# Optimization experiments

Measured on AMD Instinct MI355X. Metric: run time of the kernel, lower is better.

## Reference

```python
import jax, jax.numpy as jnp
import numpy as np

N = 256        # num_nodes
F = 256        # feature_dim
B = 32         # batch
DEG = 32       # out-degree per node -> E = N*DEG edges


def setup_inputs() -> dict:
    key = jax.random.key(0)
    k1, k2, k3, k4 = jax.random.split(key, 4)
    node_features = jax.random.normal(k1, (B, N, F), dtype=jnp.float32)
    # xavier_uniform for [N, N, F] tensor: fan_in = N*F, fan_out = N*F per torch default flattening
    limit = float(np.sqrt(6.0 / (N * F + N * F)))
    W = jax.random.uniform(k2, (N, N, F), dtype=jnp.float32, minval=-limit, maxval=limit)
    phase = jax.random.uniform(k3, (N, N), dtype=jnp.float32, minval=0.0, maxval=2.0 * np.pi)
    # topology: each node i has DEG outgoing connections (paths[i])
    src = jnp.repeat(jnp.arange(N, dtype=jnp.int64), DEG)              # [E]
    dst = jax.random.randint(k4, (N * DEG,), 0, N, dtype=jnp.int64)    # [E]
    return {"node_features": node_features, "W": W, "phase": phase, "src": src, "dst": dst}


def reference(node_features, W, phase, src, dst):
    # real(exp(i*phase)) == cos(phase); per-edge effective weight [E, F]
    eff_w = W[src, dst, :] * jnp.cos(phase[src, dst])[:, None]
    # gather source node features and scale: [B, E, F]
    signal = node_features[:, src, :] * eff_w[None, :, :]
    # scatter-add into destination nodes
    propagated = jnp.zeros_like(node_features).at[:, dst, :].add(signal)
    # normalization by out-degree of each node index (matches original indexing)
    n = node_features.shape[1]
    counts = jnp.zeros((n,), dtype=node_features.dtype).at[src].add(1.0)
    norm = jnp.maximum(counts, 1.0)
    return propagated / norm[None, :, None]
```

## Files before the change

### kernel.cpp

```cpp
#include <hip/hip_runtime.h>
#include <math.h>

#define NN 256
#define FF 256
#define BB 32
#define EE 8192


#define FGROUPS 8
#define CAP 96

__global__ __launch_bounds__(256, 4) void fused_propagate_kernel(
    const float4* __restrict__ nf4,
    const float4* __restrict__ W4,
    const float*  __restrict__ phase,
    const int*    __restrict__ dst,
    float4*       __restrict__ out4)
{
    const int fg   = blockIdx.x & (FGROUPS - 1);
    const int d    = blockIdx.x >> 3;
    const int tid  = threadIdx.x;
    const int lane = tid & 63;
    const int wv   = tid >> 6;

    __shared__ int    scnt[NN];
    __shared__ int2   lsa[CAP];
    __shared__ int    wtot[4];
    __shared__ float4 aw4[CAP * 8];

    const int4* dstq = (const int4*)dst;
    int c[8];
    #pragma unroll
    for (int i = 0; i < 8; i++) {
        const int4 v = dstq[tid + 256 * i];
        c[i] = (v.x == d) + (v.y == d) + (v.z == d) + (v.w == d);
    }
    #pragma unroll
    for (int off = 1; off < 8; off <<= 1) {
        #pragma unroll
        for (int i = 0; i < 8; i++) c[i] += __shfl_xor(c[i], off, 64);
    }
    if ((tid & 7) == 0) {
        const int g = tid >> 3;
        #pragma unroll
        for (int i = 0; i < 8; i++) scnt[g + 32 * i] = c[i];
    }
    __syncthreads();

    const int cnt = scnt[tid];
    const int ind = (cnt > 0) ? 1 : 0;

    const unsigned long long mask  = __ballot(ind);
    const int                below = __popcll(mask & ((1ULL << lane) - 1ULL));
    if (lane == 0) wtot[wv] = __popcll(mask);
    __syncthreads();

    int wbase = 0;
    #pragma unroll
    for (int w = 0; w < 4; w++) wbase += (w < wv) ? wtot[w] : 0;
    const int total = wtot[0] + wtot[1] + wtot[2] + wtot[3];

    if (ind) {
        const float a = (float)cnt * cosf(phase[tid * NN + d]) * 0.03125f;
        lsa[wbase + below] = make_int2(tid, __float_as_int(a));
    }
    const int n4 = (total + 3) & ~3;
    if (tid < n4 - total) lsa[total + tid] = make_int2(0, 0);
    __syncthreads();

    const int wrow = d * (FF / 4) + fg * 8;
    for (int slot = tid; slot < n4 * 8; slot += 256) {
        const int  e = slot >> 3, f = slot & 7;
        const int2 sa = lsa[e];
        const float a = __int_as_float(sa.y);
        float4 w = W4[sa.x * (NN * FF / 4) + wrow + f];
        w.x *= a; w.y *= a; w.z *= a; w.w *= a;
        aw4[slot] = w;
    }
    __syncthreads();

    const int myf = tid & 7;
    const int b   = tid >> 3;
    const int nfb = b * (NN * FF / 4) + fg * 8 + myf;

    float4 acc = {0.f, 0.f, 0.f, 0.f};

    if (n4 > 0) {
        int s0 = lsa[0].x, s1 = lsa[1].x, s2 = lsa[2].x, s3 = lsa[3].x;
        float4 x0 = nf4[nfb + s0 * (FF / 4)];
        float4 x1 = nf4[nfb + s1 * (FF / 4)];
        float4 x2 = nf4[nfb + s2 * (FF / 4)];
        float4 x3 = nf4[nfb + s3 * (FF / 4)];

        for (int k = 4; k < n4; k += 4) {
            const int t0 = lsa[k + 0].x, t1 = lsa[k + 1].x;
            const int t2 = lsa[k + 2].x, t3 = lsa[k + 3].x;
            const float4 y0 = nf4[nfb + t0 * (FF / 4)];
            const float4 y1 = nf4[nfb + t1 * (FF / 4)];
            const float4 y2 = nf4[nfb + t2 * (FF / 4)];
            const float4 y3 = nf4[nfb + t3 * (FF / 4)];

            {
                const float4 a0 = aw4[(k - 4) * 8 + myf];
                const float4 a1 = aw4[(k - 3) * 8 + myf];
                const float4 a2 = aw4[(k - 2) * 8 + myf];
                const float4 a3 = aw4[(k - 1) * 8 + myf];
                acc.x = fmaf(x0.x, a0.x, acc.x); acc.y = fmaf(x0.y, a0.y, acc.y);
                acc.z = fmaf(x0.z, a0.z, acc.z); acc.w = fmaf(x0.w, a0.w, acc.w);
                acc.x = fmaf(x1.x, a1.x, acc.x); acc.y = fmaf(x1.y, a1.y, acc.y);
                acc.z = fmaf(x1.z, a1.z, acc.z); acc.w = fmaf(x1.w, a1.w, acc.w);
                acc.x = fmaf(x2.x, a2.x, acc.x); acc.y = fmaf(x2.y, a2.y, acc.y);
                acc.z = fmaf(x2.z, a2.z, acc.z); acc.w = fmaf(x2.w, a2.w, acc.w);
                acc.x = fmaf(x3.x, a3.x, acc.x); acc.y = fmaf(x3.y, a3.y, acc.y);
                acc.z = fmaf(x3.z, a3.z, acc.z); acc.w = fmaf(x3.w, a3.w, acc.w);
            }
            x0 = y0; x1 = y1; x2 = y2; x3 = y3;
        }

        {
            const float4 a0 = aw4[(n4 - 4) * 8 + myf];
            const float4 a1 = aw4[(n4 - 3) * 8 + myf];
            const float4 a2 = aw4[(n4 - 2) * 8 + myf];
            const float4 a3 = aw4[(n4 - 1) * 8 + myf];
            acc.x = fmaf(x0.x, a0.x, acc.x); acc.y = fmaf(x0.y, a0.y, acc.y);
            acc.z = fmaf(x0.z, a0.z, acc.z); acc.w = fmaf(x0.w, a0.w, acc.w);
            acc.x = fmaf(x1.x, a1.x, acc.x); acc.y = fmaf(x1.y, a1.y, acc.y);
            acc.z = fmaf(x1.z, a1.z, acc.z); acc.w = fmaf(x1.w, a1.w, acc.w);
            acc.x = fmaf(x2.x, a2.x, acc.x); acc.y = fmaf(x2.y, a2.y, acc.y);
            acc.z = fmaf(x2.z, a2.z, acc.z); acc.w = fmaf(x2.w, a2.w, acc.w);
            acc.x = fmaf(x3.x, a3.x, acc.x); acc.y = fmaf(x3.y, a3.y, acc.y);
            acc.z = fmaf(x3.z, a3.z, acc.z); acc.w = fmaf(x3.w, a3.w, acc.w);
        }
    }

    out4[b * (NN * FF / 4) + d * (FF / 4) + fg * 8 + myf] = acc;
}

extern "C" void kernel_launch(void* const* d_in, const int* in_sizes, int n_in,
                              void* d_out, int out_size, void* d_ws, size_t ws_size,
                              hipStream_t stream) {
    const float* nf    = (const float*)d_in[0];
    const float* W     = (const float*)d_in[1];
    const float* phase = (const float*)d_in[2];
    const int*   dst   = (const int*)d_in[4];
    float*       out   = (float*)d_out;

    fused_propagate_kernel<<<NN * FGROUPS, 256, 0, stream>>>(
        (const float4*)nf, (const float4*)W, phase, dst, (float4*)out);
}
```

Measured before the change: 116.0 us.

## Use one 1024-thread block per destination node covering all features

Replaces the 8 feature-group blocks per destination node with a single 1024-thread block per node that handles all 256 features. Each thread now accumulates two float4 outputs, and the destination histogram, compaction and phase lookups are done once per node rather than eight times. This removes redundant scanning of the dst array and lowers block count, but grid size drops to 256 blocks and shared memory per block grows to about 96 KB. That limits occupancy and may underfill the GPU's compute units.

```diff
diff --git a/kernel.cpp b/kernel.cpp
--- a/kernel.cpp
+++ b/kernel.cpp
@@ -7,18 +7,16 @@
 #define EE 8192
 
 
-#define FGROUPS 8
 #define CAP 96
 
-__global__ __launch_bounds__(256, 4) void fused_propagate_kernel(
+__global__ __launch_bounds__(1024, 4) void fused_propagate_kernel(
     const float4* __restrict__ nf4,
     const float4* __restrict__ W4,
     const float*  __restrict__ phase,
     const int*    __restrict__ dst,
     float4*       __restrict__ out4)
 {
-    const int fg   = blockIdx.x & (FGROUPS - 1);
-    const int d    = blockIdx.x >> 3;
+    const int d    = blockIdx.x;
     const int tid  = threadIdx.x;
     const int lane = tid & 63;
     const int wv   = tid >> 6;
@@ -26,39 +24,36 @@
     __shared__ int    scnt[NN];
     __shared__ int2   lsa[CAP];
     __shared__ int    wtot[4];
-    __shared__ float4 aw4[CAP * 8];
+    __shared__ float4 aw4[CAP * 64];
 
     const int4* dstq = (const int4*)dst;
-    int c[8];
-    #pragma unroll
-    for (int i = 0; i < 8; i++) {
-        const int4 v = dstq[tid + 256 * i];
-        c[i] = (v.x == d) + (v.y == d) + (v.z == d) + (v.w == d);
-    }
+    const int4 v0 = dstq[tid];
+    const int4 v1 = dstq[tid + 1024];
+    int c0 = (v0.x == d) + (v0.y == d) + (v0.z == d) + (v0.w == d);
+    int c1 = (v1.x == d) + (v1.y == d) + (v1.z == d) + (v1.w == d);
     #pragma unroll
     for (int off = 1; off < 8; off <<= 1) {
-        #pragma unroll
-        for (int i = 0; i < 8; i++) c[i] += __shfl_xor(c[i], off, 64);
+        c0 += __shfl_xor(c0, off, 64);
+        c1 += __shfl_xor(c1, off, 64);
     }
     if ((tid & 7) == 0) {
-        const int g = tid >> 3;
-        #pragma unroll
-        for (int i = 0; i < 8; i++) scnt[g + 32 * i] = c[i];
+        scnt[tid >> 3]       = c0;
+        scnt[128 + (tid >> 3)] = c1;
     }
     __syncthreads();
 
-    const int cnt = scnt[tid];
-    const int ind = (cnt > 0) ? 1 : 0;
+    int cnt = 0, ind = 0;
+    if (tid < NN) { cnt = scnt[tid]; ind = (cnt > 0) ? 1 : 0; }
 
     const unsigned long long mask  = __ballot(ind);
     const int                below = __popcll(mask & ((1ULL << lane) - 1ULL));
-    if (lane == 0) wtot[wv] = __popcll(mask);
+    if (wv < 4 && lane == 0) wtot[wv] = __popcll(mask);
     __syncthreads();
 
+    const int total = wtot[0] + wtot[1] + wtot[2] + wtot[3];
     int wbase = 0;
     #pragma unroll
     for (int w = 0; w < 4; w++) wbase += (w < wv) ? wtot[w] : 0;
-    const int total = wtot[0] + wtot[1] + wtot[2] + wtot[3];
 
     if (ind) {
         const float a = (float)cnt * cosf(phase[tid * NN + d]) * 0.03125f;
@@ -68,72 +63,107 @@
     if (tid < n4 - total) lsa[total + tid] = make_int2(0, 0);
     __syncthreads();
 
-    const int wrow = d * (FF / 4) + fg * 8;
-    for (int slot = tid; slot < n4 * 8; slot += 256) {
-        const int  e = slot >> 3, f = slot & 7;
+    const int drow = d * (FF / 4);
+    for (int slot = tid; slot < n4 * 64; slot += 1024) {
+        const int  e = slot >> 6, f = slot & 63;
         const int2 sa = lsa[e];
         const float a = __int_as_float(sa.y);
-        float4 w = W4[sa.x * (NN * FF / 4) + wrow + f];
+        float4 w = W4[sa.x * (NN * FF / 4) + drow + f];
         w.x *= a; w.y *= a; w.z *= a; w.w *= a;
         aw4[slot] = w;
     }
     __syncthreads();
 
-    const int myf = tid & 7;
-    const int b   = tid >> 3;
-    const int nfb = b * (NN * FF / 4) + fg * 8 + myf;
+    const int b   = tid >> 5;
+    const int q   = tid & 31;
+    const int nfb = b * (NN * (FF / 4)) + q;
 
-    float4 acc = {0.f, 0.f, 0.f, 0.f};
+    float4 acc0 = {0.f, 0.f, 0.f, 0.f};
+    float4 acc1 = {0.f, 0.f, 0.f, 0.f};
 
     if (n4 > 0) {
         int s0 = lsa[0].x, s1 = lsa[1].x, s2 = lsa[2].x, s3 = lsa[3].x;
-        float4 x0 = nf4[nfb + s0 * (FF / 4)];
-        float4 x1 = nf4[nfb + s1 * (FF / 4)];
-        float4 x2 = nf4[nfb + s2 * (FF / 4)];
-        float4 x3 = nf4[nfb + s3 * (FF / 4)];
+        float4 xl0 = nf4[nfb + s0 * 64];
+        float4 xh0 = nf4[nfb + s0 * 64 + 32];
+        float4 xl1 = nf4[nfb + s1 * 64];
+        float4 xh1 = nf4[nfb + s1 * 64 + 32];
+        float4 xl2 = nf4[nfb + s2 * 64];
+        float4 xh2 = nf4[nfb + s2 * 64 + 32];
+        float4 xl3 = nf4[nfb + s3 * 64];
+        float4 xh3 = nf4[nfb + s3 * 64 + 32];
 
         for (int k = 4; k < n4; k += 4) {
             const int t0 = lsa[k + 0].x, t1 = lsa[k + 1].x;
             const int t2 = lsa[k + 2].x, t3 = lsa[k + 3].x;
-            const float4 y0 = nf4[nfb + t0 * (FF / 4)];
-            const float4 y1 = nf4[nfb + t1 * (FF / 4)];
-            const float4 y2 = nf4[nfb + t2 * (FF / 4)];
-            const float4 y3 = nf4[nfb + t3 * (FF / 4)];
+            const float4 yl0 = nf4[nfb + t0 * 64];
+            const float4 yh0 = nf4[nfb + t0 * 64 + 32];
+            const float4 yl1 = nf4[nfb + t1 * 64];
+            const float4 yh1 = nf4[nfb + t1 * 64 + 32];
+            const float4 yl2 = nf4[nfb + t2 * 64];
+            const float4 yh2 = nf4[nfb + t2 * 64 + 32];
+            const float4 yl3 = nf4[nfb + t3 * 64];
+            const float4 yh3 = nf4[nfb + t3 * 64 + 32];
 
             {
-                const float4 a0 = aw4[(k - 4) * 8 + myf];
-                const float4 a1 = aw4[(k - 3) * 8 + myf];
-                const float4 a2 = aw4[(k - 2) * 8 + myf];
-                const float4 a3 = aw4[(k - 1) * 8 + myf];
-                acc.x = fmaf(x0.x, a0.x, acc.x); acc.y = fmaf(x0.y, a0.y, acc.y);
-                acc.z = fmaf(x0.z, a0.z, acc.z); acc.w = fmaf(x0.w, a0.w, acc.w);
-                acc.x = fmaf(x1.x, a1.x, acc.x); acc.y = fmaf(x1.y, a1.y, acc.y);
-                acc.z = fmaf(x1.z, a1.z, acc.z); acc.w = fmaf(x1.w, a1.w, acc.w);
-                acc.x = fmaf(x2.x, a2.x, acc.x); acc.y = fmaf(x2.y, a2.y, acc.y);
-                acc.z = fmaf(x2.z, a2.z, acc.z); acc.w = fmaf(x2.w, a2.w, acc.w);
-                acc.x = fmaf(x3.x, a3.x, acc.x); acc.y = fmaf(x3.y, a3.y, acc.y);
-                acc.z = fmaf(x3.z, a3.z, acc.z); acc.w = fmaf(x3.w, a3.w, acc.w);
+                const float4 al0 = aw4[(k - 4) * 64 + q];
+                const float4 ah0 = aw4[(k - 4) * 64 + q + 32];
+                const float4 al1 = aw4[(k - 3) * 64 + q];
+                const float4 ah1 = aw4[(k - 3) * 64 + q + 32];
+                const float4 al2 = aw4[(k - 2) * 64 + q];
+                const float4 ah2 = aw4[(k - 2) * 64 + q + 32];
+                const float4 al3 = aw4[(k - 1) * 64 + q];
+                const float4 ah3 = aw4[(k - 1) * 64 + q + 32];
+                acc0.x = fmaf(xl0.x, al0.x, acc0.x); acc0.y = fmaf(xl0.y, al0.y, acc0.y);
+                acc0.z = fmaf(xl0.z, al0.z, acc0.z); acc0.w = fmaf(xl0.w, al0.w, acc0.w);
+                acc1.x = fmaf(xh0.x, ah0.x, acc1.x); acc1.y = fmaf(xh0.y, ah0.y, acc1.y);
+                acc1.z = fmaf(xh0.z, ah0.z, acc1.z); acc1.w = fmaf(xh0.w, ah0.w, acc1.w);
+                acc0.x = fmaf(xl1.x, al1.x, acc0.x); acc0.y = fmaf(xl1.y, al1.y, acc0.y);
+                acc0.z = fmaf(xl1.z, al1.z, acc0.z); acc0.w = fmaf(xl1.w, al1.w, acc0.w);
+                acc1.x = fmaf(xh1.x, ah1.x, acc1.x); acc1.y = fmaf(xh1.y, ah1.y, acc1.y);
+                acc1.z = fmaf(xh1.z, ah1.z, acc1.z); acc1.w = fmaf(xh1.w, ah1.w, acc1.w);
+                acc0.x = fmaf(xl2.x, al2.x, acc0.x); acc0.y = fmaf(xl2.y, al2.y, acc0.y);
+                acc0.z = fmaf(xl2.z, al2.z, acc0.z); acc0.w = fmaf(xl2.w, al2.w, acc0.w);
+                acc1.x = fmaf(xh2.x, ah2.x, acc1.x); acc1.y = fmaf(xh2.y, ah2.y, acc1.y);
+                acc1.z = fmaf(xh2.z, ah2.z, acc1.z); acc1.w = fmaf(xh2.w, ah2.w, acc1.w);
+                acc0.x = fmaf(xl3.x, al3.x, acc0.x); acc0.y = fmaf(xl3.y, al3.y, acc0.y);
+                acc0.z = fmaf(xl3.z, al3.z, acc0.z); acc0.w = fmaf(xl3.w, al3.w, acc0.w);
+                acc1.x = fmaf(xh3.x, ah3.x, acc1.x); acc1.y = fmaf(xh3.y, ah3.y, acc1.y);
+                acc1.z = fmaf(xh3.z, ah3.z, acc1.z); acc1.w = fmaf(xh3.w, ah3.w, acc1.w);
             }
-            x0 = y0; x1 = y1; x2 = y2; x3 = y3;
+            xl0 = yl0; xh0 = yh0; xl1 = yl1; xh1 = yh1;
+            xl2 = yl2; xh2 = yh2; xl3 = yl3; xh3 = yh3;
         }
 
         {
-            const float4 a0 = aw4[(n4 - 4) * 8 + myf];
-            const float4 a1 = aw4[(n4 - 3) * 8 + myf];
-            const float4 a2 = aw4[(n4 - 2) * 8 + myf];
-            const float4 a3 = aw4[(n4 - 1) * 8 + myf];
-            acc.x = fmaf(x0.x, a0.x, acc.x); acc.y = fmaf(x0.y, a0.y, acc.y);
-            acc.z = fmaf(x0.z, a0.z, acc.z); acc.w = fmaf(x0.w, a0.w, acc.w);
-            acc.x = fmaf(x1.x, a1.x, acc.x); acc.y = fmaf(x1.y, a1.y, acc.y);
-            acc.z = fmaf(x1.z, a1.z, acc.z); acc.w = fmaf(x1.w, a1.w, acc.w);
-            acc.x = fmaf(x2.x, a2.x, acc.x); acc.y = fmaf(x2.y, a2.y, acc.y);
-            acc.z = fmaf(x2.z, a2.z, acc.z); acc.w = fmaf(x2.w, a2.w, acc.w);
-            acc.x = fmaf(x3.x, a3.x, acc.x); acc.y = fmaf(x3.y, a3.y, acc.y);
-            acc.z = fmaf(x3.z, a3.z, acc.z); acc.w = fmaf(x3.w, a3.w, acc.w);
+            const float4 al0 = aw4[(n4 - 4) * 64 + q];
+            const float4 ah0 = aw4[(n4 - 4) * 64 + q + 32];
+            const float4 al1 = aw4[(n4 - 3) * 64 + q];
+            const float4 ah1 = aw4[(n4 - 3) * 64 + q + 32];
+            const float4 al2 = aw4[(n4 - 2) * 64 + q];
+            const float4 ah2 = aw4[(n4 - 2) * 64 + q + 32];
+            const float4 al3 = aw4[(n4 - 1) * 64 + q];
+            const float4 ah3 = aw4[(n4 - 1) * 64 + q + 32];
+            acc0.x = fmaf(xl0.x, al0.x, acc0.x); acc0.y = fmaf(xl0.y, al0.y, acc0.y);
+            acc0.z = fmaf(xl0.z, al0.z, acc0.z); acc0.w = fmaf(xl0.w, al0.w, acc0.w);
+            acc1.x = fmaf(xh0.x, ah0.x, acc1.x); acc1.y = fmaf(xh0.y, ah0.y, acc1.y);
+            acc1.z = fmaf(xh0.z, ah0.z, acc1.z); acc1.w = fmaf(xh0.w, ah0.w, acc1.w);
+            acc0.x = fmaf(xl1.x, al1.x, acc0.x); acc0.y = fmaf(xl1.y, al1.y, acc0.y);
+            acc0.z = fmaf(xl1.z, al1.z, acc0.z); acc0.w = fmaf(xl1.w, al1.w, acc0.w);
+            acc1.x = fmaf(xh1.x, ah1.x, acc1.x); acc1.y = fmaf(xh1.y, ah1.y, acc1.y);
+            acc1.z = fmaf(xh1.z, ah1.z, acc1.z); acc1.w = fmaf(xh1.w, ah1.w, acc1.w);
+            acc0.x = fmaf(xl2.x, al2.x, acc0.x); acc0.y = fmaf(xl2.y, al2.y, acc0.y);
+            acc0.z = fmaf(xl2.z, al2.z, acc0.z); acc0.w = fmaf(xl2.w, al2.w, acc0.w);
+            acc1.x = fmaf(xh2.x, ah2.x, acc1.x); acc1.y = fmaf(xh2.y, ah2.y, acc1.y);
+            acc1.z = fmaf(xh2.z, ah2.z, acc1.z); acc1.w = fmaf(xh2.w, ah2.w, acc1.w);
+            acc0.x = fmaf(xl3.x, al3.x, acc0.x); acc0.y = fmaf(xl3.y, al3.y, acc0.y);
+            acc0.z = fmaf(xl3.z, al3.z, acc0.z); acc0.w = fmaf(xl3.w, al3.w, acc0.w);
+            acc1.x = fmaf(xh3.x, ah3.x, acc1.x); acc1.y = fmaf(xh3.y, ah3.y, acc1.y);
+            acc1.z = fmaf(xh3.z, ah3.z, acc1.z); acc1.w = fmaf(xh3.w, ah3.w, acc1.w);
         }
     }
 
-    out4[b * (NN * FF / 4) + d * (FF / 4) + fg * 8 + myf] = acc;
+    out4[b * (NN * (FF / 4)) + drow + q]      = acc0;
+    out4[b * (NN * (FF / 4)) + drow + q + 32] = acc1;
 }
 
 extern "C" void kernel_launch(void* const* d_in, const int* in_sizes, int n_in,
@@ -145,6 +175,6 @@
     const int*   dst   = (const int*)d_in[4];
     float*       out   = (float*)d_out;
 
-    fused_propagate_kernel<<<NN * FGROUPS, 256, 0, stream>>>(
+    fused_propagate_kernel<<<NN, 1024, 0, stream>>>(
         (const float4*)nf, (const float4*)W, phase, dst, (float4*)out);
 }
```

Result: no change. 114.9 us (-1.0%).

## Stage node features in LDS per feature quad and process 64 destinations per block

Applied to the files above, without the earlier changes.

Each block now owns one float4 feature column across all batches and nodes, loading the full B×N slice of node features into LDS once and reusing it for 64 destination nodes. Edge counts are built with a packed-byte LDS histogram via atomics, and per-destination source/coef lists are compacted per wave. W is streamed directly from global memory with a one-step register prefetch instead of being prescaled in LDS. This cuts redundant global reads of node features, at the cost of 128KB LDS per block, 1024-thread blocks and only 256 blocks, and the per-destination source list is truncated at CAP entries.

```diff
diff --git a/kernel.cpp b/kernel.cpp
--- a/kernel.cpp
+++ b/kernel.cpp
@@ -5,135 +5,161 @@
 #define FF 256
 #define BB 32
 #define EE 8192
+#define F4  (FF / 4)
+#define NF4 (NN * F4)
 
 
-#define FGROUPS 8
-#define CAP 96
+#define CAP 80
 
-__global__ __launch_bounds__(256, 4) void fused_propagate_kernel(
+#define CONSUME4()                                                             \
+    {                                                                          \
+        const float4 xA = nf_lds[sA * 32 + b];                                 \
+        const float4 xB = nf_lds[sB * 32 + b];                                 \
+        const float4 xC = nf_lds[sC * 32 + b];                                 \
+        const float4 xD = nf_lds[sD * 32 + b];                                 \
+        float4 aw;                                                             \
+        aw.x = a4.x * wA.x; aw.y = a4.x * wA.y;                                \
+        aw.z = a4.x * wA.z; aw.w = a4.x * wA.w;                                \
+        acc.x = fmaf(xA.x, aw.x, acc.x); acc.y = fmaf(xA.y, aw.y, acc.y);      \
+        acc.z = fmaf(xA.z, aw.z, acc.z); acc.w = fmaf(xA.w, aw.w, acc.w);      \
+        aw.x = a4.y * wB.x; aw.y = a4.y * wB.y;                                \
+        aw.z = a4.y * wB.z; aw.w = a4.y * wB.w;                                \
+        acc.x = fmaf(xB.x, aw.x, acc.x); acc.y = fmaf(xB.y, aw.y, acc.y);      \
+        acc.z = fmaf(xB.z, aw.z, acc.z); acc.w = fmaf(xB.w, aw.w, acc.w);      \
+        aw.x = a4.z * wC.x; aw.y = a4.z * wC.y;                                \
+        aw.z = a4.z * wC.z; aw.w = a4.z * wC.w;                                \
+        acc.x = fmaf(xC.x, aw.x, acc.x); acc.y = fmaf(xC.y, aw.y, acc.y);      \
+        acc.z = fmaf(xC.z, aw.z, acc.z); acc.w = fmaf(xC.w, aw.w, acc.w);      \
+        aw.x = a4.w * wD.x; aw.y = a4.w * wD.y;                                \
+        aw.z = a4.w * wD.z; aw.w = a4.w * wD.w;                                \
+        acc.x = fmaf(xD.x, aw.x, acc.x); acc.y = fmaf(xD.y, aw.y, acc.y);      \
+        acc.z = fmaf(xD.z, aw.z, acc.z); acc.w = fmaf(xD.w, aw.w, acc.w);      \
+    }
+
+__global__ __launch_bounds__(1024, 4) void fused_propagate_kernel(
     const float4* __restrict__ nf4,
     const float4* __restrict__ W4,
     const float*  __restrict__ phase,
     const int*    __restrict__ dst,
     float4*       __restrict__ out4)
 {
-    const int fg   = blockIdx.x & (FGROUPS - 1);
-    const int d    = blockIdx.x >> 3;
-    const int tid  = threadIdx.x;
-    const int lane = tid & 63;
-    const int wv   = tid >> 6;
+    const int bid = blockIdx.x;
+    const int ql  = bid >> 6;
+    const int dq  = (bid >> 4) & 3;
+    const int qg  = bid & 15;
+    const int q   = qg * 4 + ql;
+    const int d0  = dq * 64;
 
-    __shared__ int    scnt[NN];
-    __shared__ int2   lsa[CAP];
-    __shared__ int    wtot[4];
-    __shared__ float4 aw4[CAP * 8];
+    const int t    = threadIdx.x;
+    const int lane = t & 63;
+    const int wv   = t >> 6;
 
-    const int4* dstq = (const int4*)dst;
-    int c[8];
-    #pragma unroll
-    for (int i = 0; i < 8; i++) {
-        const int4 v = dstq[tid + 256 * i];
-        c[i] = (v.x == d) + (v.y == d) + (v.z == d) + (v.w == d);
-    }
-    #pragma unroll
-    for (int off = 1; off < 8; off <<= 1) {
-        #pragma unroll
-        for (int i = 0; i < 8; i++) c[i] += __shfl_xor(c[i], off, 64);
-    }
-    if ((tid & 7) == 0) {
-        const int g = tid >> 3;
-        #pragma unroll
-        for (int i = 0; i < 8; i++) scnt[g + 32 * i] = c[i];
+    __shared__ float4 nf_lds[BB * NN];
+    __shared__ __align__(16) unsigned char s_list[64 * CAP];
+    __shared__ __align__(16) float         a_list[64 * CAP];
+    __shared__ int llen[64];
+
+    const float4* pp = nf4 + (t & 31) * NF4 + (t >> 5) * F4 + q;
+    const float4 r0 = pp[0 * 2048], r1 = pp[1 * 2048];
+    const float4 r2 = pp[2 * 2048], r3 = pp[3 * 2048];
+    const float4 r4 = pp[4 * 2048], r5 = pp[5 * 2048];
+    const float4 r6 = pp[6 * 2048], r7 = pp[7 * 2048];
+
+    unsigned int* hist = (unsigned int*)nf_lds;
+    hist[t] = 0u; hist[t + 1024] = 0u; hist[t + 2048] = 0u; hist[t + 3072] = 0u;
+    __syncthreads();
+    {
+        const int4* dstq = (const int4*)dst;
+        const int4 v0 = dstq[t];
+        const int4 v1 = dstq[t + 1024];
+        const int  s0 = t >> 3;
+        const int  s1 = 128 + (t >> 3);
+#define CNT_EDGE(dv, sv)                                                       \
+        if (((dv) >> 6) == dq) {                                               \
+            const int dl_ = (dv) & 63;                                         \
+            atomicAdd(&hist[(sv) * 16 + (dl_ >> 2)], 1u << ((dl_ & 3) * 8));   \
+        }
+        CNT_EDGE(v0.x, s0) CNT_EDGE(v0.y, s0) CNT_EDGE(v0.z, s0) CNT_EDGE(v0.w, s0)
+        CNT_EDGE(v1.x, s1) CNT_EDGE(v1.y, s1) CNT_EDGE(v1.z, s1) CNT_EDGE(v1.w, s1)
+#undef CNT_EDGE
     }
     __syncthreads();
 
-    const int cnt = scnt[tid];
-    const int ind = (cnt > 0) ? 1 : 0;
-
-    const unsigned long long mask  = __ballot(ind);
-    const int                below = __popcll(mask & ((1ULL << lane) - 1ULL));
-    if (lane == 0) wtot[wv] = __popcll(mask);
-    __syncthreads();
-
-    int wbase = 0;
-    #pragma unroll
-    for (int w = 0; w < 4; w++) wbase += (w < wv) ? wtot[w] : 0;
-    const int total = wtot[0] + wtot[1] + wtot[2] + wtot[3];
-
-    if (ind) {
-        const float a = (float)cnt * cosf(phase[tid * NN + d]) * 0.03125f;
-        lsa[wbase + below] = make_int2(tid, __float_as_int(a));
-    }
-    const int n4 = (total + 3) & ~3;
-    if (tid < n4 - total) lsa[total + tid] = make_int2(0, 0);
-    __syncthreads();
-
-    const int wrow = d * (FF / 4) + fg * 8;
-    for (int slot = tid; slot < n4 * 8; slot += 256) {
-        const int  e = slot >> 3, f = slot & 7;
-        const int2 sa = lsa[e];
-        const float a = __int_as_float(sa.y);
-        float4 w = W4[sa.x * (NN * FF / 4) + wrow + f];
-        w.x *= a; w.y *= a; w.z *= a; w.w *= a;
-        aw4[slot] = w;
+    for (int dd = 0; dd < 4; ++dd) {
+        const int dl = wv * 4 + dd;
+        const int d  = d0 + dl;
+        int base = 0;
+        for (int chunk = 0; chunk < 4; ++chunk) {
+            const int s   = chunk * 64 + lane;
+            const int cnt = (int)((hist[s * 16 + (dl >> 2)] >> ((dl & 3) * 8)) & 0xFFu);
+            const unsigned long long m = __ballot(cnt > 0);
+            if (cnt > 0) {
+                const int pos = base + __popcll(m & ((1ULL << lane) - 1ULL));
+                if (pos < CAP) {
+                    s_list[dl * CAP + pos] = (unsigned char)s;
+                    a_list[dl * CAP + pos] =
+                        (float)cnt * cosf(phase[s * NN + d]) * 0.03125f;
+                }
+            }
+            base += __popcll(m);
+        }
+        const int n4 = (base + 3) & ~3;
+        if (lane < n4 - base) {
+            s_list[dl * CAP + base + lane] = 0;
+            a_list[dl * CAP + base + lane] = 0.0f;
+        }
+        if (lane == 0) llen[dl] = base;
     }
     __syncthreads();
 
-    const int myf = tid & 7;
-    const int b   = tid >> 3;
-    const int nfb = b * (NN * FF / 4) + fg * 8 + myf;
+    nf_lds[t]        = r0; nf_lds[t + 1024] = r1;
+    nf_lds[t + 2048] = r2; nf_lds[t + 3072] = r3;
+    nf_lds[t + 4096] = r4; nf_lds[t + 5120] = r5;
+    nf_lds[t + 6144] = r6; nf_lds[t + 7168] = r7;
+    __syncthreads();
 
-    float4 acc = {0.f, 0.f, 0.f, 0.f};
+    const int b = t & 31;
+    const int g = t >> 5;
 
-    if (n4 > 0) {
-        int s0 = lsa[0].x, s1 = lsa[1].x, s2 = lsa[2].x, s3 = lsa[3].x;
-        float4 x0 = nf4[nfb + s0 * (FF / 4)];
-        float4 x1 = nf4[nfb + s1 * (FF / 4)];
-        float4 x2 = nf4[nfb + s2 * (FF / 4)];
-        float4 x3 = nf4[nfb + s3 * (FF / 4)];
+    for (int dp = 0; dp < 2; ++dp) {
+        const int dl   = g + 32 * dp;
+        const int d    = d0 + dl;
+        const int lb   = dl * CAP;
+        const int n4   = (llen[dl] + 3) & ~3;
+        const int wrow = d * F4 + q;
 
-        for (int k = 4; k < n4; k += 4) {
-            const int t0 = lsa[k + 0].x, t1 = lsa[k + 1].x;
-            const int t2 = lsa[k + 2].x, t3 = lsa[k + 3].x;
-            const float4 y0 = nf4[nfb + t0 * (FF / 4)];
-            const float4 y1 = nf4[nfb + t1 * (FF / 4)];
-            const float4 y2 = nf4[nfb + t2 * (FF / 4)];
-            const float4 y3 = nf4[nfb + t3 * (FF / 4)];
+        float4 acc = {0.f, 0.f, 0.f, 0.f};
 
-            {
-                const float4 a0 = aw4[(k - 4) * 8 + myf];
-                const float4 a1 = aw4[(k - 3) * 8 + myf];
-                const float4 a2 = aw4[(k - 2) * 8 + myf];
-                const float4 a3 = aw4[(k - 1) * 8 + myf];
-                acc.x = fmaf(x0.x, a0.x, acc.x); acc.y = fmaf(x0.y, a0.y, acc.y);
-                acc.z = fmaf(x0.z, a0.z, acc.z); acc.w = fmaf(x0.w, a0.w, acc.w);
-                acc.x = fmaf(x1.x, a1.x, acc.x); acc.y = fmaf(x1.y, a1.y, acc.y);
-                acc.z = fmaf(x1.z, a1.z, acc.z); acc.w = fmaf(x1.w, a1.w, acc.w);
-                acc.x = fmaf(x2.x, a2.x, acc.x); acc.y = fmaf(x2.y, a2.y, acc.y);
-                acc.z = fmaf(x2.z, a2.z, acc.z); acc.w = fmaf(x2.w, a2.w, acc.w);
-                acc.x = fmaf(x3.x, a3.x, acc.x); acc.y = fmaf(x3.y, a3.y, acc.y);
-                acc.z = fmaf(x3.z, a3.z, acc.z); acc.w = fmaf(x3.w, a3.w, acc.w);
+        if (n4 > 0) {
+            unsigned int s4 = *(const unsigned int*)&s_list[lb];
+            float4       a4 = *(const float4*)&a_list[lb];
+            int sA = (int)(s4 & 255u), sB = (int)((s4 >> 8) & 255u);
+            int sC = (int)((s4 >> 16) & 255u), sD = (int)(s4 >> 24);
+            float4 wA = W4[sA * NF4 + wrow];
+            float4 wB = W4[sB * NF4 + wrow];
+            float4 wC = W4[sC * NF4 + wrow];
+            float4 wD = W4[sD * NF4 + wrow];
+
+            for (int k = 4; k < n4; k += 4) {
+                const unsigned int s4n = *(const unsigned int*)&s_list[lb + k];
+                const float4       a4n = *(const float4*)&a_list[lb + k];
+                const int sE = (int)(s4n & 255u), sF_ = (int)((s4n >> 8) & 255u);
+                const int sG = (int)((s4n >> 16) & 255u), sH = (int)(s4n >> 24);
+                const float4 wE = W4[sE * NF4 + wrow];
+                const float4 wF = W4[sF_ * NF4 + wrow];
+                const float4 wG = W4[sG * NF4 + wrow];
+                const float4 wH = W4[sH * NF4 + wrow];
+
+                CONSUME4()
+
+                sA = sE; sB = sF_; sC = sG; sD = sH;
+                a4 = a4n; wA = wE; wB = wF; wC = wG; wD = wH;
             }
-            x0 = y0; x1 = y1; x2 = y2; x3 = y3;
+            CONSUME4()
         }
 
-        {
-            const float4 a0 = aw4[(n4 - 4) * 8 + myf];
-            const float4 a1 = aw4[(n4 - 3) * 8 + myf];
-            const float4 a2 = aw4[(n4 - 2) * 8 + myf];
-            const float4 a3 = aw4[(n4 - 1) * 8 + myf];
-            acc.x = fmaf(x0.x, a0.x, acc.x); acc.y = fmaf(x0.y, a0.y, acc.y);
-            acc.z = fmaf(x0.z, a0.z, acc.z); acc.w = fmaf(x0.w, a0.w, acc.w);
-            acc.x = fmaf(x1.x, a1.x, acc.x); acc.y = fmaf(x1.y, a1.y, acc.y);
-            acc.z = fmaf(x1.z, a1.z, acc.z); acc.w = fmaf(x1.w, a1.w, acc.w);
-            acc.x = fmaf(x2.x, a2.x, acc.x); acc.y = fmaf(x2.y, a2.y, acc.y);
-            acc.z = fmaf(x2.z, a2.z, acc.z); acc.w = fmaf(x2.w, a2.w, acc.w);
-            acc.x = fmaf(x3.x, a3.x, acc.x); acc.y = fmaf(x3.y, a3.y, acc.y);
-            acc.z = fmaf(x3.z, a3.z, acc.z); acc.w = fmaf(x3.w, a3.w, acc.w);
-        }
+        out4[b * NF4 + wrow] = acc;
     }
-
-    out4[b * (NN * FF / 4) + d * (FF / 4) + fg * 8 + myf] = acc;
 }
 
 extern "C" void kernel_launch(void* const* d_in, const int* in_sizes, int n_in,
@@ -145,6 +171,6 @@
     const int*   dst   = (const int*)d_in[4];
     float*       out   = (float*)d_out;
 
-    fused_propagate_kernel<<<NN * FGROUPS, 256, 0, stream>>>(
+    fused_propagate_kernel<<<256, 1024, 0, stream>>>(
         (const float4*)nf, (const float4*)W, phase, dst, (float4*)out);
 }
```

Result: slower. 133.3 us (+14.9%).

## Restructure blocks to cover full feature row with half-batch per block

Applied to the files above, without the earlier changes.

Changes the work decomposition from 2048 blocks of 256 threads (one 32-float feature slice per block) to 512 blocks of 1024 threads, each covering all 256 features for half the batch. Each block now stages the full W row slice once per destination instead of per feature group, which cuts the redundant dst scans and phase/cos work. Source indices are packed as bytes so one shared load yields four sources. The trade-offs are a much larger shared buffer (CAP*64 float4s, 64 KiB), which limits occupancy, and CAP is lowered to 64, which risks overflow if any in-degree set exceeds 64 distinct sources.

```diff
diff --git a/kernel.cpp b/kernel.cpp
--- a/kernel.cpp
+++ b/kernel.cpp
@@ -5,106 +5,112 @@
 #define FF 256
 #define BB 32
 #define EE 8192
+#define F4  (FF / 4)
+#define NF4 (NN * F4)
 
 
-#define FGROUPS 8
-#define CAP 96
+#define CAP 64
 
-__global__ __launch_bounds__(256, 4) void fused_propagate_kernel(
+__global__ __launch_bounds__(1024, 8) void fused_propagate_kernel(
     const float4* __restrict__ nf4,
     const float4* __restrict__ W4,
     const float*  __restrict__ phase,
     const int*    __restrict__ dst,
     float4*       __restrict__ out4)
 {
-    const int fg   = blockIdx.x & (FGROUPS - 1);
-    const int d    = blockIdx.x >> 3;
-    const int tid  = threadIdx.x;
-    const int lane = tid & 63;
-    const int wv   = tid >> 6;
+    const int bid = blockIdx.x;
+    const int d   = bid >> 1;
+    const int h   = bid & 1;
 
-    __shared__ int    scnt[NN];
-    __shared__ int2   lsa[CAP];
-    __shared__ int    wtot[4];
-    __shared__ float4 aw4[CAP * 8];
+    const int t    = threadIdx.x;
+    const int lane = t & 63;
+    const int wv   = t >> 6;
+
+    __shared__ int          scnt[NN];
+    __shared__ unsigned int s_pk[CAP / 4];
+    __shared__ float        a_list[CAP];
+    __shared__ int          wtot[4];
+    __shared__ float4       aw4[CAP * 64];
 
     const int4* dstq = (const int4*)dst;
-    int c[8];
-    #pragma unroll
-    for (int i = 0; i < 8; i++) {
-        const int4 v = dstq[tid + 256 * i];
-        c[i] = (v.x == d) + (v.y == d) + (v.z == d) + (v.w == d);
-    }
+    const int4 v0 = dstq[t];
+    const int4 v1 = dstq[t + 1024];
+    int c0 = (v0.x == d) + (v0.y == d) + (v0.z == d) + (v0.w == d);
+    int c1 = (v1.x == d) + (v1.y == d) + (v1.z == d) + (v1.w == d);
     #pragma unroll
     for (int off = 1; off < 8; off <<= 1) {
-        #pragma unroll
-        for (int i = 0; i < 8; i++) c[i] += __shfl_xor(c[i], off, 64);
+        c0 += __shfl_xor(c0, off, 64);
+        c1 += __shfl_xor(c1, off, 64);
     }
-    if ((tid & 7) == 0) {
-        const int g = tid >> 3;
-        #pragma unroll
-        for (int i = 0; i < 8; i++) scnt[g + 32 * i] = c[i];
+    if ((t & 7) == 0) {
+        scnt[t >> 3]         = c0;
+        scnt[128 + (t >> 3)] = c1;
     }
     __syncthreads();
 
-    const int cnt = scnt[tid];
-    const int ind = (cnt > 0) ? 1 : 0;
+    int cnt = 0, ind = 0;
+    if (t < NN) { cnt = scnt[t]; ind = (cnt > 0) ? 1 : 0; }
 
     const unsigned long long mask  = __ballot(ind);
     const int                below = __popcll(mask & ((1ULL << lane) - 1ULL));
-    if (lane == 0) wtot[wv] = __popcll(mask);
+    if (wv < 4 && lane == 0) wtot[wv] = __popcll(mask);
     __syncthreads();
 
+    const int total = wtot[0] + wtot[1] + wtot[2] + wtot[3];
     int wbase = 0;
     #pragma unroll
     for (int w = 0; w < 4; w++) wbase += (w < wv) ? wtot[w] : 0;
-    const int total = wtot[0] + wtot[1] + wtot[2] + wtot[3];
 
+    unsigned char* s8w = (unsigned char*)s_pk;
     if (ind) {
-        const float a = (float)cnt * cosf(phase[tid * NN + d]) * 0.03125f;
-        lsa[wbase + below] = make_int2(tid, __float_as_int(a));
+        const float a = (float)cnt * cosf(phase[t * NN + d]) * 0.03125f;
+        const int pos = wbase + below;
+        s8w[pos]    = (unsigned char)t;
+        a_list[pos] = a;
     }
     const int n4 = (total + 3) & ~3;
-    if (tid < n4 - total) lsa[total + tid] = make_int2(0, 0);
+    if (t < n4 - total) {
+        s8w[total + t]    = 0;
+        a_list[total + t] = 0.0f;
+    }
     __syncthreads();
 
-    const int wrow = d * (FF / 4) + fg * 8;
-    for (int slot = tid; slot < n4 * 8; slot += 256) {
-        const int  e = slot >> 3, f = slot & 7;
-        const int2 sa = lsa[e];
-        const float a = __int_as_float(sa.y);
-        float4 w = W4[sa.x * (NN * FF / 4) + wrow + f];
+    const int drow = d * F4;
+    const unsigned char* s8 = (const unsigned char*)s_pk;
+    for (int slot = t; slot < (n4 << 6); slot += 1024) {
+        const int   e = slot >> 6, f = slot & 63;
+        const float a = a_list[e];
+        float4 w = W4[(int)s8[e] * NF4 + drow + f];
         w.x *= a; w.y *= a; w.z *= a; w.w *= a;
         aw4[slot] = w;
     }
     __syncthreads();
 
-    const int myf = tid & 7;
-    const int b   = tid >> 3;
-    const int nfb = b * (NN * FF / 4) + fg * 8 + myf;
+    const int q = t & 63;
+    const int b = h * 16 + (t >> 6);
+    const float4* nfb = nf4 + b * NF4 + q;
 
     float4 acc = {0.f, 0.f, 0.f, 0.f};
 
     if (n4 > 0) {
-        int s0 = lsa[0].x, s1 = lsa[1].x, s2 = lsa[2].x, s3 = lsa[3].x;
-        float4 x0 = nf4[nfb + s0 * (FF / 4)];
-        float4 x1 = nf4[nfb + s1 * (FF / 4)];
-        float4 x2 = nf4[nfb + s2 * (FF / 4)];
-        float4 x3 = nf4[nfb + s3 * (FF / 4)];
+        const unsigned int su = s_pk[0];
+        float4 x0 = nfb[((su      ) & 255u) * 64];
+        float4 x1 = nfb[((su >>  8) & 255u) * 64];
+        float4 x2 = nfb[((su >> 16) & 255u) * 64];
+        float4 x3 = nfb[((su >> 24)       ) * 64];
 
         for (int k = 4; k < n4; k += 4) {
-            const int t0 = lsa[k + 0].x, t1 = lsa[k + 1].x;
-            const int t2 = lsa[k + 2].x, t3 = lsa[k + 3].x;
-            const float4 y0 = nf4[nfb + t0 * (FF / 4)];
-            const float4 y1 = nf4[nfb + t1 * (FF / 4)];
-            const float4 y2 = nf4[nfb + t2 * (FF / 4)];
-            const float4 y3 = nf4[nfb + t3 * (FF / 4)];
+            const unsigned int sn = s_pk[k >> 2];
+            const float4 y0 = nfb[((sn      ) & 255u) * 64];
+            const float4 y1 = nfb[((sn >>  8) & 255u) * 64];
+            const float4 y2 = nfb[((sn >> 16) & 255u) * 64];
+            const float4 y3 = nfb[((sn >> 24)       ) * 64];
 
             {
-                const float4 a0 = aw4[(k - 4) * 8 + myf];
-                const float4 a1 = aw4[(k - 3) * 8 + myf];
-                const float4 a2 = aw4[(k - 2) * 8 + myf];
-                const float4 a3 = aw4[(k - 1) * 8 + myf];
+                const float4 a0 = aw4[(k - 4) * 64 + q];
+                const float4 a1 = aw4[(k - 3) * 64 + q];
+                const float4 a2 = aw4[(k - 2) * 64 + q];
+                const float4 a3 = aw4[(k - 1) * 64 + q];
                 acc.x = fmaf(x0.x, a0.x, acc.x); acc.y = fmaf(x0.y, a0.y, acc.y);
                 acc.z = fmaf(x0.z, a0.z, acc.z); acc.w = fmaf(x0.w, a0.w, acc.w);
                 acc.x = fmaf(x1.x, a1.x, acc.x); acc.y = fmaf(x1.y, a1.y, acc.y);
@@ -118,10 +124,10 @@
         }
 
         {
-            const float4 a0 = aw4[(n4 - 4) * 8 + myf];
-            const float4 a1 = aw4[(n4 - 3) * 8 + myf];
-            const float4 a2 = aw4[(n4 - 2) * 8 + myf];
-            const float4 a3 = aw4[(n4 - 1) * 8 + myf];
+            const float4 a0 = aw4[(n4 - 4) * 64 + q];
+            const float4 a1 = aw4[(n4 - 3) * 64 + q];
+            const float4 a2 = aw4[(n4 - 2) * 64 + q];
+            const float4 a3 = aw4[(n4 - 1) * 64 + q];
             acc.x = fmaf(x0.x, a0.x, acc.x); acc.y = fmaf(x0.y, a0.y, acc.y);
             acc.z = fmaf(x0.z, a0.z, acc.z); acc.w = fmaf(x0.w, a0.w, acc.w);
             acc.x = fmaf(x1.x, a1.x, acc.x); acc.y = fmaf(x1.y, a1.y, acc.y);
@@ -133,7 +139,7 @@
         }
     }
 
-    out4[b * (NN * FF / 4) + d * (FF / 4) + fg * 8 + myf] = acc;
+    out4[b * NF4 + drow + q] = acc;
 }
 
 extern "C" void kernel_launch(void* const* d_in, const int* in_sizes, int n_in,
@@ -145,6 +151,6 @@
     const int*   dst   = (const int*)d_in[4];
     float*       out   = (float*)d_out;
 
-    fused_propagate_kernel<<<NN * FGROUPS, 256, 0, stream>>>(
+    fused_propagate_kernel<<<512, 1024, 0, stream>>>(
         (const float4*)nf, (const float4*)W, phase, dst, (float4*)out);
 }
```

New measurement: 117.9 us. No clear change (+1.6%).
